# Performance work log

Measured on AMD Instinct MI355X. Metric: run time of the kernel, lower is better.

## Reference

```python
import jax, jax.numpy as jnp
import numpy as np

B, N, A, D = 256, 64, 16, 256  # rollout threads, n_agents, action_dim, inputs_dim
NEG_INF = -1e10


def setup_inputs() -> dict:
    key = jax.random.key(0)
    k0, k1, k2, k3 = jax.random.split(key, 4)
    x = jax.random.normal(k0, (B, D), dtype=jnp.float32)
    # adj[i, j, p] = 1 iff p is a parent of j in graph i; strict lower triangle -> DAG
    adj = jax.random.randint(k1, (B, N, N), 0, 2, dtype=jnp.int32)
    adj = adj * jnp.tril(jnp.ones((N, N), jnp.int32), -1)
    available_actions = jnp.ones((B, A), dtype=jnp.float32)
    father_weights = jax.random.normal(k2, (N,), dtype=jnp.float32)  # nn.Parameter(ones) in torch
    W = jax.random.normal(k3, (A, D + A * N * N), dtype=jnp.float32) * 0.02  # Categorical head
    b = jnp.zeros((A,), dtype=jnp.float32)
    return {"x": x, "adj": adj, "available_actions": available_actions,
            "father_weights": father_weights, "W": W, "b": b}


def reference(x, adj, available_actions, father_weights, W, b):
    Bsz = x.shape[0]
    # In the source, actions=[0]*n_agents is never updated, so each parent block is
    # onehot(0) scaled by father_action_weights[parent]; topological order is irrelevant.
    fa = adj.astype(x.dtype) * father_weights[None, None, :]          # [B, N, N]
    onehot0 = jnp.zeros((A,), x.dtype).at[0].set(1.0)
    father = fa[..., None] * onehot0                                   # [B, N, N, A]
    father_flat = father.reshape(Bsz, N, N * A)                        # father_action_lst_outer
    x_ = jnp.concatenate([x, father_flat.reshape(Bsz, -1)], axis=-1)  # [B, D + A*N*N]
    logits = x_ @ W.T + b                                              # [B, A]
    logits = jnp.where(available_actions > 0, logits, NEG_INF)
    logp_all = jax.nn.log_softmax(logits, axis=-1)
    actions = jnp.argmax(logits, axis=-1)[:, None]                     # deterministic mode
    action_log_probs = jnp.take_along_axis(logp_all, actions, axis=-1)  # [B, 1]
    return actions, action_log_probs, father_flat.reshape(Bsz, N * N * A)
```

## Files before the change

### kernel.cpp

```cpp
#include <hip/hip_runtime.h>
#include <hip/hip_bf16.h>

#define BB 256
#define NN 64
#define AA 16
#define DD 256
#define WCOLS (DD + AA * NN * NN)
#define NK (NN * NN)

__global__ __launch_bounds__(256) void actg_logits_kernel(
    const float* __restrict__ x, const int* __restrict__ adj,
    const float* __restrict__ avail, const float* __restrict__ fw,
    const float* __restrict__ W, const float* __restrict__ bias,
    float* __restrict__ out_actions, float* __restrict__ out_logp)
{
    const int b = blockIdx.x;
    const int t = threadIdx.x;

    __shared__ float s_fw[NN];
    __shared__ float s_part[4][AA];
    __shared__ float s_logits[AA];

    if (t < NN) s_fw[t] = fw[t];
    __syncthreads();

    float acc[AA];
#pragma unroll
    for (int a = 0; a < AA; ++a) acc[a] = 0.f;

    const int* adjb = adj + b * NK;
    for (int it = 0; it < NK / 256; ++it) {
        const int k = it * 256 + t;
        const int av = adjb[k];
        if (av) {
            const float val = s_fw[k & (NN - 1)];
            const float* wp = W + DD + k * AA;
#pragma unroll
            for (int a = 0; a < AA; ++a)
                acc[a] += val * wp[a * WCOLS];
        }
    }

    {
        const float xv = x[b * DD + t];
        const float* wp = W + t;
#pragma unroll
        for (int a = 0; a < AA; ++a)
            acc[a] += xv * wp[a * WCOLS];
    }

#pragma unroll
    for (int a = 0; a < AA; ++a) {
        float v = acc[a];
#pragma unroll
        for (int off = 32; off > 0; off >>= 1)
            v += __shfl_down(v, off, 64);
        acc[a] = v;
    }
    const int wave = t >> 6;
    if ((t & 63) == 0) {
#pragma unroll
        for (int a = 0; a < AA; ++a) s_part[wave][a] = acc[a];
    }
    __syncthreads();

    if (t < AA) {
        float v = s_part[0][t] + s_part[1][t] + s_part[2][t] + s_part[3][t]
                + bias[t];
        v = (avail[b * AA + t] > 0.f) ? v : -1e10f;
        s_logits[t] = v;
    }
    __syncthreads();

    if (t == 0) {
        float m = s_logits[0];
        int am = 0;
#pragma unroll
        for (int a = 1; a < AA; ++a) {
            const float v = s_logits[a];
            if (v > m) { m = v; am = a; }
        }
        float s = 0.f;
#pragma unroll
        for (int a = 0; a < AA; ++a) s += expf(s_logits[a] - m);
        out_actions[b] = (float)am;
        out_logp[b]    = -logf(s);
    }
}

__global__ __launch_bounds__(256) void actg_father_kernel(
    const int* __restrict__ adj, const float* __restrict__ fw,
    float4* __restrict__ out)
{
    const int g  = blockIdx.x * blockDim.x + threadIdx.x;
    const int bk = g >> 2;
    const int a4 = g & 3;
    const float av = (float)adj[bk];
    const float v  = av * fw[bk & (NN - 1)];
    const float val = (a4 == 0) ? v : 0.f;
    out[g] = make_float4(val, 0.f, 0.f, 0.f);
}

extern "C" void kernel_launch(void* const* d_in, const int* in_sizes, int n_in,
                              void* d_out, int out_size, void* d_ws, size_t ws_size,
                              hipStream_t stream) {
    const float* x     = (const float*)d_in[0];
    const int*   adj   = (const int*)  d_in[1];
    const float* avail = (const float*)d_in[2];
    const float* fw    = (const float*)d_in[3];
    const float* W     = (const float*)d_in[4];
    const float* bias  = (const float*)d_in[5];

    float* out = (float*)d_out;
    float*  out_actions = out;
    float*  out_logp    = out + BB;
    float4* out_father  = (float4*)(out + 2 * BB);

    actg_logits_kernel<<<BB, 256, 0, stream>>>(
        x, adj, avail, fw, W, bias, out_actions, out_logp);

    const int total_f4 = BB * NK * (AA / 4);
    actg_father_kernel<<<total_f4 / 256, 256, 0, stream>>>(
        adj, fw, out_father);
}
```

Measured before the change: 111.4 us.

## Compact strided W columns into a dense transposed buffer before logits

Adds a pre-pass kernel that gathers the only W columns that can be nonzero-weighted (the onehot(0) column per parent slot) into a compact [NK, A] buffer in workspace. The logits kernel then reads adj as int4 and fetches the 16 weights per slot as four float4 loads instead of 16 widely strided scalar loads. This is meant to replace scattered DRAM reads across a ~4 MB-strided W with a small contiguous 256 KB table shared by all blocks. The cost is an extra kernel launch and a workspace write each call.

```diff
diff --git a/kernel.cpp b/kernel.cpp
--- a/kernel.cpp
+++ b/kernel.cpp
@@ -8,10 +8,20 @@
 #define WCOLS (DD + AA * NN * NN)
 #define NK (NN * NN)
 
+__global__ __launch_bounds__(256) void actg_compact_kernel(
+    const float* __restrict__ W, float* __restrict__ Wc)
+{
+    const int t = blockIdx.x * 256 + threadIdx.x;
+    const int a = t >> 12;
+    const int k = t & (NK - 1);
+    Wc[k * AA + a] = W[a * WCOLS + DD + k * AA];
+}
+
 __global__ __launch_bounds__(256) void actg_logits_kernel(
     const float* __restrict__ x, const int* __restrict__ adj,
     const float* __restrict__ avail, const float* __restrict__ fw,
     const float* __restrict__ W, const float* __restrict__ bias,
+    const float* __restrict__ Wc,
     float* __restrict__ out_actions, float* __restrict__ out_logp)
 {
     const int b = blockIdx.x;
@@ -28,18 +38,36 @@
 #pragma unroll
     for (int a = 0; a < AA; ++a) acc[a] = 0.f;
 
-    const int* adjb = adj + b * NK;
-    for (int it = 0; it < NK / 256; ++it) {
-        const int k = it * 256 + t;
-        const int av = adjb[k];
-        if (av) {
-            const float val = s_fw[k & (NN - 1)];
-            const float* wp = W + DD + k * AA;
+    const int4*   adjb4 = (const int4*)(adj + b * NK);
+    const float4* Wc4   = (const float4*)Wc;
+
+#define PROC(AVQ, KQ)                                              \
+    if (AVQ) {                                                     \
+        const float  val = s_fw[(KQ) & (NN - 1)];                  \
+        const float4 w0  = Wc4[(KQ) * 4 + 0];                      \
+        const float4 w1  = Wc4[(KQ) * 4 + 1];                      \
+        const float4 w2  = Wc4[(KQ) * 4 + 2];                      \
+        const float4 w3  = Wc4[(KQ) * 4 + 3];                      \
+        acc[0]  += val * w0.x;  acc[1]  += val * w0.y;             \
+        acc[2]  += val * w0.z;  acc[3]  += val * w0.w;             \
+        acc[4]  += val * w1.x;  acc[5]  += val * w1.y;             \
+        acc[6]  += val * w1.z;  acc[7]  += val * w1.w;             \
+        acc[8]  += val * w2.x;  acc[9]  += val * w2.y;             \
+        acc[10] += val * w2.z;  acc[11] += val * w2.w;             \
+        acc[12] += val * w3.x;  acc[13] += val * w3.y;             \
+        acc[14] += val * w3.z;  acc[15] += val * w3.w;             \
+    }
+
 #pragma unroll
-            for (int a = 0; a < AA; ++a)
-                acc[a] += val * wp[a * WCOLS];
-        }
+    for (int it = 0; it < NK / (256 * 4); ++it) {
+        const int4 av = adjb4[it * 256 + t];
+        const int  k0 = (it * 256 + t) * 4;
+        PROC(av.x, k0 + 0)
+        PROC(av.y, k0 + 1)
+        PROC(av.z, k0 + 2)
+        PROC(av.w, k0 + 3)
     }
+#undef PROC
 
     {
         const float xv = x[b * DD + t];
@@ -116,8 +144,12 @@
     float*  out_logp    = out + BB;
     float4* out_father  = (float4*)(out + 2 * BB);
 
+    float* Wc = (float*)d_ws;
+
+    actg_compact_kernel<<<NK * AA / 256, 256, 0, stream>>>(W, Wc);
+
     actg_logits_kernel<<<BB, 256, 0, stream>>>(
-        x, adj, avail, fw, W, bias, out_actions, out_logp);
+        x, adj, avail, fw, W, bias, Wc, out_actions, out_logp);
 
     const int total_f4 = BB * NK * (AA / 4);
     actg_father_kernel<<<total_f4 / 256, 256, 0, stream>>>(
```

Result: faster. 101.4 us (-9.0%).
